# Performance work log

Measured on AMD Instinct MI355X. Metric: run time of the kernel, lower is better.

## Reference

```python
import jax, jax.numpy as jnp
import numpy as np

B, L, V, E, H, C, OUT = 128, 256, 50000, 300, 128, 4, 2
D = 2 * H  # features_size == sequence_max_len (required by the conv kernel width)
FS = (2, 3, 4, 5)


def _p(key, shape, s=0.05):
    return (jax.random.normal(key, shape) * s).astype(jnp.float32)


def setup_inputs() -> dict:
    key = jax.random.key(0)
    ks = jax.random.split(key, 32)
    emb = _p(ks[0], (V, E)).at[0].set(0.0)  # padding_idx=0
    inp = {
        'utterance': jax.random.randint(ks[1], (B, L), 1, V, dtype=jnp.int32),
        'seq_lengths': jnp.full((B,), L, dtype=jnp.int32),
        'emb': emb,
        'w_ih0': _p(ks[2], (2, 3 * H, E)), 'w_hh0': _p(ks[3], (2, 3 * H, H)),
        'b_ih0': _p(ks[4], (2, 3 * H)), 'b_hh0': _p(ks[5], (2, 3 * H)),
        'w_ih1': _p(ks[6], (2, 3 * H, 2 * H)), 'w_hh1': _p(ks[7], (2, 3 * H, H)),
        'b_ih1': _p(ks[8], (2, 3 * H)), 'b_hh1': _p(ks[9], (2, 3 * H)),
        'att_w': _p(ks[10], (C, D, D)), 'att_b': _p(ks[11], (C,)),
        'att_wv2': _p(ks[12], (C, D, D)), 'att_bv': _p(ks[13], (C, D)),
        'att_wv1': _p(ks[14], (C, D)),
        'fc_w': _p(ks[15], (OUT, sum(FS))), 'fc_b': _p(ks[16], (OUT,)),
    }
    for i, fs in enumerate(FS):
        inp[f'conv_w{i}'] = _p(ks[17 + 2 * i], (fs, C, fs, L))
        inp[f'conv_b{i}'] = _p(ks[18 + 2 * i], (fs,))
    return inp


def _gru_dir(x, w_ih, w_hh, b_ih, b_hh, reverse):
    # x: (B,T,in) -> (B,T,H); PyTorch GRU cell equations, eval mode (no dropout)
    gx = jnp.einsum('bti,gi->btg', x, w_ih) + b_ih  # (B,T,3H)

    def step(h, gxt):
        gh = h @ w_hh.T + b_hh
        xr, xz, xn = jnp.split(gxt, 3, axis=-1)
        hr, hz, hn = jnp.split(gh, 3, axis=-1)
        r = jax.nn.sigmoid(xr + hr)
        z = jax.nn.sigmoid(xz + hz)
        n = jnp.tanh(xn + r * hn)
        h = (1.0 - z) * n + z * h
        return h, h

    h0 = jnp.zeros((x.shape[0], w_hh.shape[1]), x.dtype)
    _, ys = jax.lax.scan(step, h0, jnp.swapaxes(gx, 0, 1), reverse=reverse)
    return jnp.swapaxes(ys, 0, 1)


def _bigru_layer(x, w_ih, w_hh, b_ih, b_hh):
    f = _gru_dir(x, w_ih[0], w_hh[0], b_ih[0], b_hh[0], False)
    b = _gru_dir(x, w_ih[1], w_hh[1], b_ih[1], b_hh[1], True)
    return jnp.concatenate([f, b], axis=-1)


def _forward(utterance, emb, w_ih0, w_hh0, b_ih0, b_hh0, w_ih1, w_hh1, b_ih1, b_hh1,
             att_w, att_b, att_wv2, att_bv, att_wv1, conv_params, fc_w, fc_b):
    x = emb[utterance]                                   # (B,L,E)
    x = _bigru_layer(x, w_ih0, w_hh0, b_ih0, b_hh0)      # (B,L,2H)
    x = _bigru_layer(x, w_ih1, w_hh1, b_ih1, b_hh1)      # (B,L,D)
    # --- AMCNN attention, vectorized over channels c ---
    mat = jnp.einsum('bld,cde->cble', x, att_w)          # mat_l per channel (C,B,L,D)
    # M_l[b,i,j] = <inputs[b,i], mat_l[b,j]> + b_l  (the torch tile/sum written as matmul)
    M = jnp.einsum('bid,cbjd->cbij', x, mat) + att_b[:, None, None, None]
    a = jax.nn.softmax(jnp.tanh(M).sum(axis=3), axis=2)  # scalar attention (C,B,L)
    g = jax.nn.sigmoid(jnp.einsum('bld,cde->cble', x, att_wv2) + att_bv[:, None, None, :])
    aa = jax.nn.softmax(jnp.einsum('cble,ce->cbl', g, att_wv1), axis=2)  # vector attn (C,B,L)
    new = jnp.einsum('cbl,bld->cbd', aa, x)              # weighted sum, broadcast over L
    Cf = a[..., None] * x[None] + new[:, :, None, :]     # (C,B,L,D)
    Cf = jnp.transpose(Cf, (1, 0, 2, 3))                 # (B,C,L,D)
    # --- conv blocks: Conv2d(k=(fs,L)) + ReLU + MaxPool((L-fs+1,1)) + Flatten ---
    pools = []
    for w, bi in conv_params:
        y = jax.lax.conv_general_dilated(Cf, w, (1, 1), 'VALID',
                                         dimension_numbers=('NCHW', 'OIHW', 'NCHW'))
        y = jax.nn.relu(y + bi[None, :, None, None])     # (B,fs,L-fs+1,1)
        pools.append(y.max(axis=(2, 3)))                 # (B,fs)
    feats = jnp.concatenate(pools, axis=-1)              # (B,sum(FS))
    return feats @ fc_w.T + fc_b                         # (B,OUT)


def reference(utterance, seq_lengths, emb, w_ih0, w_hh0, b_ih0, b_hh0,
              w_ih1, w_hh1, b_ih1, b_hh1, att_w, att_b, att_wv2, att_bv, att_wv1,
              conv_w0, conv_b0, conv_w1, conv_b1, conv_w2, conv_b2, conv_w3, conv_b3,
              fc_w, fc_b):
    # seq_lengths are all == L, so pack/pad_packed is an identity here
    conv_params = ((conv_w0, conv_b0), (conv_w1, conv_b1), (conv_w2, conv_b2), (conv_w3, conv_b3))
    return _forward(utterance, emb, w_ih0, w_hh0, b_ih0, b_hh0, w_ih1, w_hh1, b_ih1, b_hh1,
                    att_w, att_b, att_wv2, att_bv, att_wv1, conv_params, fc_w, fc_b)
```

## Files before the change

kernel.cpp:

```cpp
#include <hip/hip_runtime.h>
#include <hip/hip_bf16.h>
#include <hip/hip_fp16.h>

#define Bn  128
#define Ln  256
#define En  300
#define Hn  128
#define Cn  4
#define Dn  256
#define G3n 384
#define BLn (Bn * Ln)

typedef __hip_bfloat16 bf16;
typedef short s16x8 __attribute__((ext_vector_type(8)));
typedef float f32x4 __attribute__((ext_vector_type(4)));
typedef _Float16 h16x2 __attribute__((ext_vector_type(2)));

__device__ __forceinline__ float ldf(const float* p) { return *p; }
__device__ __forceinline__ float ldf(const bf16* p)  { return __bfloat162float(*p); }
__device__ __forceinline__ void stf(float* p, float v) { *p = v; }
__device__ __forceinline__ void stf(bf16* p, float v)  { *p = __float2bfloat16(v); }

__device__ __forceinline__ ushort f2bf(float f) {
    bf16 h = __float2bfloat16(f);
    return *reinterpret_cast<ushort*>(&h);
}
__device__ __forceinline__ float bfu(ushort x) {
    unsigned t = ((unsigned)x) << 16;
    return __builtin_bit_cast(float, t);
}

#if __has_builtin(__builtin_amdgcn_fdot2)
__device__ __forceinline__ float dot2f(h16x2 w, h16x2 h, float c) {
    return __builtin_amdgcn_fdot2(w, h, c, false);
}
#else
__device__ __forceinline__ float dot2f(h16x2 w, h16x2 h, float c) {
    return fmaf((float)w[0], (float)h[0], fmaf((float)w[1], (float)h[1], c));
}
#endif
#define BCH(x) __builtin_bit_cast(h16x2, x)

__device__ __forceinline__ float rdl(float v, int l) {
    return __builtin_bit_cast(float,
        __builtin_amdgcn_readlane(__builtin_bit_cast(int, v), l));
}

__device__ __forceinline__ float4 ld4f(const float* p) { return *(const float4*)p; }
__device__ __forceinline__ float4 ld4f(const bf16* p) {
    ushort4 u = *(const ushort4*)p;
    return make_float4(bfu(u.x), bfu(u.y), bfu(u.z), bfu(u.w));
}

template<class AT, class WTp, class OT, bool GATHER, int SM>
__global__ __launch_bounds__(256)
void gemm_mfma(const AT* __restrict__ A, const WTp* __restrict__ W,
               const float* __restrict__ bias, OT* __restrict__ Cout,
               const int* __restrict__ gidx, int M, int N, int K)
{
    __shared__ ushort Asm[128 * 40];
    __shared__ ushort Bsm[128 * 40];
    const int bm = blockIdx.y * 128, bn = blockIdx.x * 128;
    const int tid = threadIdx.x;
    const int lane = tid & 63, w = tid >> 6, wr = w >> 1, wc = w & 1;

    const AT* arow[4];
    const WTp* brow[4];
#pragma unroll
    for (int u = 0; u < 4; ++u) {
        const int idx = tid + u * 256;
        const int m = idx >> 3;
        arow[u] = A + (size_t)(GATHER ? gidx[bm + m] : (bm + m)) * K;
        brow[u] = W + (size_t)(bn + m) * K;
    }

    f32x4 acc[4][4] = {};
    const int nkt = (K + 31) >> 5;
    for (int kt = 0; kt < nkt; ++kt) {
        const int k0 = kt << 5;
#pragma unroll
        for (int u = 0; u < 4; ++u) {
            const int idx = tid + u * 256;
            const int m = idx >> 3, kq = idx & 7;
            const int kb = k0 + kq * 4;
            float4 v, q;
            if (kb + 4 <= K) {
                v = ld4f(arow[u] + kb);
                q = ld4f(brow[u] + kb);
            } else {
                v.x = kb + 0 < K ? ldf(&arow[u][kb + 0]) : 0.f;
                v.y = kb + 1 < K ? ldf(&arow[u][kb + 1]) : 0.f;
                v.z = kb + 2 < K ? ldf(&arow[u][kb + 2]) : 0.f;
                v.w = kb + 3 < K ? ldf(&arow[u][kb + 3]) : 0.f;
                q.x = kb + 0 < K ? ldf(&brow[u][kb + 0]) : 0.f;
                q.y = kb + 1 < K ? ldf(&brow[u][kb + 1]) : 0.f;
                q.z = kb + 2 < K ? ldf(&brow[u][kb + 2]) : 0.f;
                q.w = kb + 3 < K ? ldf(&brow[u][kb + 3]) : 0.f;
            }
            *(ushort4*)&Asm[m * 40 + kq * 4] =
                make_ushort4(f2bf(v.x), f2bf(v.y), f2bf(v.z), f2bf(v.w));
            *(ushort4*)&Bsm[m * 40 + kq * 4] =
                make_ushort4(f2bf(q.x), f2bf(q.y), f2bf(q.z), f2bf(q.w));
        }
        __syncthreads();
        s16x8 af[4], bfr[4];
#pragma unroll
        for (int t = 0; t < 4; ++t) {
            af[t]  = *(const s16x8*)&Asm[(wr * 64 + t * 16 + (lane & 15)) * 40 + (lane >> 4) * 8];
            bfr[t] = *(const s16x8*)&Bsm[(wc * 64 + t * 16 + (lane & 15)) * 40 + (lane >> 4) * 8];
        }
#pragma unroll
        for (int mf = 0; mf < 4; ++mf)
#pragma unroll
            for (int nf = 0; nf < 4; ++nf)
                acc[mf][nf] = __builtin_amdgcn_mfma_f32_16x16x32_bf16(
                    af[mf], bfr[nf], acc[mf][nf], 0, 0, 0);
        __syncthreads();
    }

#pragma unroll
    for (int mf = 0; mf < 4; ++mf)
#pragma unroll
        for (int nf = 0; nf < 4; ++nf) {
            const int col = bn + wc * 64 + nf * 16 + (lane & 15);
            const float bv_ = bias ? bias[col] : 0.f;
#pragma unroll
            for (int i = 0; i < 4; ++i) {
                const int row = bm + wr * 64 + mf * 16 + (lane >> 4) * 4 + i;
                const float v = acc[mf][nf][i] + bv_;
                if (SM == 1)
                    stf(&Cout[((size_t)(row >> 8) * N + col) * 256 + (row & 255)], v);
                else
                    stf(&Cout[(size_t)row * N + col], v);
            }
        }
}

__global__ __launch_bounds__(768, 1)
void gru_scan_v10(const bf16* __restrict__ gx, const float* __restrict__ w_hh,
                  const float* __restrict__ b_hh, bf16* __restrict__ out)
{
    const int b = blockIdx.x, dir = blockIdx.y;
    const int t = threadIdx.x;
    const int half = t >= 384 ? 1 : 0;
    const int r = t - 384 * half;
    const int lane = t & 63;
    __shared__ __align__(16) ushort wl[384 * 136];
    __shared__ __align__(16) ushort hp16[128];
    __shared__ float h_sh[128];
    __shared__ float part[384];
    __shared__ float rs[128], zs[128], gxn[128], ghn[128];

    const float* wbase = w_hh + (size_t)dir * G3n * Hn;
    for (int idx = t; idx < G3n * 64; idx += 768) {
        const int row = idx >> 6, k2 = idx & 63;
        const float2 v = *(const float2*)(wbase + row * Hn + 2 * k2);
        h16x2 p; p[0] = (_Float16)v.x; p[1] = (_Float16)v.y;
        *(h16x2*)&wl[row * 136 + 2 * k2] = p;
    }
    if (t < 128) { hp16[t] = 0; h_sh[t] = 0.f; }
    const float bh = b_hh[dir * G3n + r];
    __syncthreads();

    const size_t g0 = (size_t)b * Ln * 768 + dir * G3n + r
                      + (dir ? (size_t)(Ln - 1) * 768 : 0);
    const long gstep = dir ? -768L : 768L;
    float gcur = 0.f, gnx = 0.f;
    if (!half) { gcur = ldf(&gx[g0]); gnx = ldf(&gx[g0 + gstep]); }

    const ushort* wrow = &wl[r * 136 + half * 64];

    for (int s = 0; s < Ln; ++s) {
        const int tt = dir ? (Ln - 1 - s) : s;
        float gn2 = 0.f;
        if (!half && s + 2 < Ln) gn2 = ldf(&gx[g0 + (long)(s + 2) * gstep]);

        const float4 hown = *(const float4*)&hp16[half * 64 + (lane & 7) * 8];

        float a0 = 0.f, a1 = 0.f, a2 = 0.f, a3 = 0.f;
#pragma unroll
        for (int j = 0; j < 8; ++j) {
            const float4 wv = *(const float4*)&wrow[8 * j];
            a0 = dot2f(BCH(wv.x), BCH(rdl(hown.x, j)), a0);
            a1 = dot2f(BCH(wv.y), BCH(rdl(hown.y, j)), a1);
            a2 = dot2f(BCH(wv.z), BCH(rdl(hown.z, j)), a2);
            a3 = dot2f(BCH(wv.w), BCH(rdl(hown.w, j)), a3);
        }
        const float acc = (a0 + a1) + (a2 + a3);
        if (half) part[r] = acc;
        __syncthreads();

        if (!half) {
            const float tot = acc + part[r] + bh;
            if (r < 128)      rs[r]       = 1.f / (1.f + expf(-(gcur + tot)));
            else if (r < 256) zs[r - 128] = 1.f / (1.f + expf(-(gcur + tot)));
            else { gxn[r - 256] = gcur; ghn[r - 256] = tot; }
        }
        __syncthreads();

        if (t < 128) {
            const int j = t;
            const float nn = tanhf(gxn[j] + rs[j] * ghn[j]);
            const float hnew = (1.f - zs[j]) * nn + zs[j] * h_sh[j];
            h_sh[j] = hnew;
            const _Float16 hf = (_Float16)hnew;
            hp16[j] = __builtin_bit_cast(ushort, hf);
            out[((size_t)b * Ln + tt) * Dn + dir * Hn + j] = __float2bfloat16(hnew);
        }
        __syncthreads();
        if (!half) { gcur = gnx; gnx = gn2; }
    }
}

__global__ __launch_bounds__(256)
void attn_score_mfma(const bf16* __restrict__ x, const bf16* __restrict__ matb,
                     const float* __restrict__ attb, float* __restrict__ sout)
{
    const int it = blockIdx.x, b = blockIdx.y, c = blockIdx.z;
    const bf16* A  = x + ((size_t)b * 256 + it * 128) * 256;
    const bf16* Bm = matb + (size_t)b * 256 * 1024 + c * 256;
    __shared__ ushort Xs[128 * 40];
    __shared__ ushort Ms[128 * 40];
    const int tid = threadIdx.x, lane = tid & 63, w = tid >> 6;
    const float bc = attb[c];
    float psum[2][4] = {};

    for (int jt = 0; jt < 2; ++jt) {
        f32x4 acc[2][8] = {};
        for (int kt = 0; kt < 8; ++kt) {
            const int k0 = kt << 5;
#pragma unroll
            for (int u = 0; u < 2; ++u) {
                const int idx = tid + u * 256;
                const int m = idx >> 2, q = idx & 3;
                *(s16x8*)&Xs[m * 40 + q * 8] =
                    *(const s16x8*)&A[(size_t)m * 256 + k0 + q * 8];
                *(s16x8*)&Ms[m * 40 + q * 8] =
                    *(const s16x8*)&Bm[(size_t)(jt * 128 + m) * 1024 + k0 + q * 8];
            }
            __syncthreads();
            s16x8 af[2], bfr[8];
#pragma unroll
            for (int t = 0; t < 2; ++t)
                af[t] = *(const s16x8*)&Xs[(w * 32 + t * 16 + (lane & 15)) * 40 + (lane >> 4) * 8];
#pragma unroll
            for (int t = 0; t < 8; ++t)
                bfr[t] = *(const s16x8*)&Ms[(t * 16 + (lane & 15)) * 40 + (lane >> 4) * 8];
#pragma unroll
            for (int mf = 0; mf < 2; ++mf)
#pragma unroll
                for (int nf = 0; nf < 8; ++nf)
                    acc[mf][nf] = __builtin_amdgcn_mfma_f32_16x16x32_bf16(
                        af[mf], bfr[nf], acc[mf][nf], 0, 0, 0);
            __syncthreads();
        }
#pragma unroll
        for (int mf = 0; mf < 2; ++mf)
#pragma unroll
            for (int nf = 0; nf < 8; ++nf)
#pragma unroll
                for (int i = 0; i < 4; ++i)
                    psum[mf][i] += tanhf(acc[mf][nf][i] + bc);
    }

#pragma unroll
    for (int mf = 0; mf < 2; ++mf)
#pragma unroll
        for (int i = 0; i < 4; ++i) {
            float v = psum[mf][i];
            v += __shfl_xor(v, 1); v += __shfl_xor(v, 2);
            v += __shfl_xor(v, 4); v += __shfl_xor(v, 8);
            if ((lane & 15) == 0)
                sout[(size_t)c * BLn + b * 256 + it * 128 + w * 32 + mf * 16 + (lane >> 4) * 4 + i] = v;
        }
}

__global__ __launch_bounds__(256)
void gv_reduce(const bf16* __restrict__ gv, const float* __restrict__ bv,
               const float* __restrict__ wv1, float* __restrict__ al)
{
    const int row = blockIdx.x * 4 + (threadIdx.x >> 6);
    const int c = blockIdx.y;
    const int l = threadIdx.x & 63;
    const ushort4 u = *(const ushort4*)&gv[(size_t)row * 1024 + c * 256 + l * 4];
    const float4 bb = *(const float4*)(bv + c * Dn + l * 4);
    const float4 w  = *(const float4*)(wv1 + c * Dn + l * 4);
    float s = w.x / (1.f + expf(-(bfu(u.x) + bb.x)))
            + w.y / (1.f + expf(-(bfu(u.y) + bb.y)))
            + w.z / (1.f + expf(-(bfu(u.z) + bb.z)))
            + w.w / (1.f + expf(-(bfu(u.w) + bb.w)));
#pragma unroll
    for (int m = 1; m < 64; m <<= 1) s += __shfl_xor(s, m);
    if (l == 0) al[(size_t)c * BLn + row] = s;
}

__global__ void transpose256(const float* __restrict__ src, bf16* __restrict__ dst)
{
    const float* s = src + (size_t)blockIdx.x * 65536;
    bf16* d = dst + (size_t)blockIdx.x * 65536;
    __shared__ float t[32][33];
    const int tx = threadIdx.x & 31, ty8 = threadIdx.x >> 5;
    for (int bi = 0; bi < 8; ++bi)
        for (int bj = 0; bj < 8; ++bj) {
            __syncthreads();
            for (int r = ty8; r < 32; r += 8)
                t[r][tx] = s[(size_t)(bi * 32 + r) * 256 + bj * 32 + tx];
            __syncthreads();
            for (int r = ty8; r < 32; r += 8)
                stf(&d[(size_t)(bj * 32 + r) * 256 + bi * 32 + tx], t[tx][r]);
        }
}

__global__ void softmax256(const float* __restrict__ in, float* __restrict__ out)
{
    __shared__ float red[256];
    const int row = blockIdx.x, t = threadIdx.x;
    const float v = in[(size_t)row * 256 + t];
    red[t] = v; __syncthreads();
    for (int off = 128; off; off >>= 1) {
        if (t < off) red[t] = fmaxf(red[t], red[t + off]);
        __syncthreads();
    }
    const float mx = red[0]; __syncthreads();
    const float e = expf(v - mx);
    red[t] = e; __syncthreads();
    for (int off = 128; off; off >>= 1) {
        if (t < off) red[t] += red[t + off];
        __syncthreads();
    }
    out[(size_t)row * 256 + t] = e / red[0];
}

__global__ __launch_bounds__(256)
void weighted_sum_kernel(const float* __restrict__ aa,
                         const bf16* __restrict__ x,
                         float* __restrict__ outnew)
{
    const int b = blockIdx.x, d = threadIdx.x;
    __shared__ float w4[4][Ln];
    for (int i = d; i < 4 * Ln; i += 256)
        w4[i >> 8][i & 255] = aa[((size_t)(i >> 8) * Bn + b) * Ln + (i & 255)];
    __syncthreads();
    float a0 = 0.f, a1 = 0.f, a2 = 0.f, a3 = 0.f;
    for (int l = 0; l < Ln; ++l) {
        const float xv = ldf(&x[((size_t)b * Ln + l) * Dn + d]);
        a0 += w4[0][l] * xv; a1 += w4[1][l] * xv;
        a2 += w4[2][l] * xv; a3 += w4[3][l] * xv;
    }
    outnew[((size_t)0 * Bn + b) * Dn + d] = a0;
    outnew[((size_t)1 * Bn + b) * Dn + d] = a1;
    outnew[((size_t)2 * Bn + b) * Dn + d] = a2;
    outnew[((size_t)3 * Bn + b) * Dn + d] = a3;
}

__global__ void wpack_fill(const float* __restrict__ w0, const float* __restrict__ w1,
                           const float* __restrict__ w2, const float* __restrict__ w3,
                           float* __restrict__ wp)
{
    const int f = blockIdx.x;
    if (f < 4) {
        const int cnt[4]  = {4096, 9216, 16384, 25600};
        const int boff[4] = {0, 4096, 13312, 29696};
        const float* src = f == 0 ? w0 : f == 1 ? w1 : f == 2 ? w2 : w3;
        for (int i = threadIdx.x; i < cnt[f]; i += blockDim.x)
            wp[boff[f] + i] = src[i];
    } else {
        for (int i = threadIdx.x; i < 65536 - 55296; i += blockDim.x)
            wp[55296 + i] = 0.f;
    }
}

__global__ __launch_bounds__(256)
void nwd_kernel(const float* __restrict__ nw, const float* __restrict__ wp,
                float* __restrict__ nwd)
{
    const int b = blockIdx.x;
    __shared__ float ns[4][256];
    for (int i = threadIdx.x; i < 1024; i += 256)
        ns[i >> 8][i & 255] = nw[((size_t)((i >> 8) * Bn + b) << 8) + (i & 255)];
    __syncthreads();
    const int row = threadIdx.x;
    if (row < 216) {
        int f, base;
        if (row < 16)       { f = 0; base = 0; }
        else if (row < 52)  { f = 1; base = 16; }
        else if (row < 116) { f = 2; base = 52; }
        else                { f = 3; base = 116; }
        const int fs = f + 2, local = row - base;
        const int c = (local / fs) & 3;
        const float* wr = wp + (size_t)row * 256;
        float acc = 0.f;
        for (int k = 0; k < 256; ++k) acc += ns[c][k] * wr[k];
        nwd[b * 256 + row] = acc;
    }
}

__global__ __launch_bounds__(256)
void conv_combine(const float* __restrict__ xwT, const float* __restrict__ a,
                  const float* __restrict__ nwd, const float* __restrict__ cb,
                  float* __restrict__ pool, int fs, int base, int poff)
{
    const int b = blockIdx.x, tid = threadIdx.x;
    __shared__ float ash[4][256];
    __shared__ float basev[5];
    __shared__ float red[256];
    for (int i = tid; i < 1024; i += 256)
        ash[i >> 8][i & 255] = a[((size_t)((i >> 8) * Bn + b) << 8) + (i & 255)];
    if (tid < fs) {
        float s = cb[tid];
        for (int c = 0; c < 4; ++c)
            for (int kh = 0; kh < fs; ++kh)
                s += nwd[b * 256 + base + (tid * 4 + c) * fs + kh];
        basev[tid] = s;
    }
    __syncthreads();
    const int ni = Ln - fs + 1;
    const float* xb = xwT + ((size_t)b << 16);
    for (int o = 0; o < fs; ++o) {
        float best = 0.f;
        if (tid < ni) {
            float acc = basev[o];
            for (int c = 0; c < 4; ++c)
                for (int kh = 0; kh < fs; ++kh) {
                    const int row = base + (o * 4 + c) * fs + kh;
                    acc += ash[c][tid + kh] * xb[(row << 8) + tid + kh];
                }
            best = fmaxf(acc, 0.f);
        }
        red[tid] = best; __syncthreads();
        for (int off = 128; off; off >>= 1) {
            if (tid < off) red[tid] = fmaxf(red[tid], red[tid + off]);
            __syncthreads();
        }
        if (tid == 0) pool[b * 14 + poff + o] = red[0];
        __syncthreads();
    }
}

__global__ void fc_kernel(const float* __restrict__ pool, const float* __restrict__ fw,
                          const float* __restrict__ fb, float* __restrict__ out)
{
    const int i = threadIdx.x;
    const int b = i >> 1, o = i & 1;
    float acc = fb[o];
#pragma unroll
    for (int f = 0; f < 14; ++f) acc += pool[b * 14 + f] * fw[o * 14 + f];
    out[i] = acc;
}

extern "C" void kernel_launch(void* const* d_in, const int* in_sizes, int n_in,
                              void* d_out, int out_size, void* d_ws, size_t ws_size,
                              hipStream_t stream)
{
    const int*   utt    = (const int*)  d_in[0];
    const float* emb    = (const float*)d_in[2];
    const float* w_ih0  = (const float*)d_in[3];
    const float* w_hh0  = (const float*)d_in[4];
    const float* b_ih0  = (const float*)d_in[5];
    const float* b_hh0  = (const float*)d_in[6];
    const float* w_ih1  = (const float*)d_in[7];
    const float* w_hh1  = (const float*)d_in[8];
    const float* b_ih1  = (const float*)d_in[9];
    const float* b_hh1  = (const float*)d_in[10];
    const float* att_w  = (const float*)d_in[11];
    const float* att_b  = (const float*)d_in[12];
    const float* att_wv2= (const float*)d_in[13];
    const float* att_bv = (const float*)d_in[14];
    const float* att_wv1= (const float*)d_in[15];
    const float* fc_w   = (const float*)d_in[16];
    const float* fc_b   = (const float*)d_in[17];
    const float* cw[4] = {(const float*)d_in[18], (const float*)d_in[20],
                          (const float*)d_in[22], (const float*)d_in[24]};
    const float* cb[4] = {(const float*)d_in[19], (const float*)d_in[21],
                          (const float*)d_in[23], (const float*)d_in[25]};

    float* ws = (float*)d_ws;
    bf16*  GX   = (bf16*)ws;
    bf16*  H1   = (bf16*)(ws + 12582912);
    bf16*  H2   = (bf16*)(ws + 16777216);
    bf16*  WT   = (bf16*)(ws + 20971520);
    float* WP   = ws + 20971520 + 131072;
    float* S    = WP + 65536;
    float* Aa   = S + 131072;
    float* AL   = Aa + 131072;
    float* AAa  = AL + 131072;
    float* NEW_ = AAa + 131072;
    float* NWD  = NEW_ + 131072;
    float* POOL = NWD + 32768;
    bf16*  MATB = (bf16*)ws;
    float* XWT  = ws;

    gemm_mfma<float, float, bf16, true, 0><<<dim3(6, 256), 256, 0, stream>>>(
        emb, w_ih0, b_ih0, GX, utt, BLn, 768, En);
    gru_scan_v10<<<dim3(Bn, 2), 768, 0, stream>>>(GX, w_hh0, b_hh0, H1);
    gemm_mfma<bf16, float, bf16, false, 0><<<dim3(6, 256), 256, 0, stream>>>(
        H1, w_ih1, b_ih1, GX, nullptr, BLn, 768, Dn);
    gru_scan_v10<<<dim3(Bn, 2), 768, 0, stream>>>(GX, w_hh1, b_hh1, H2);

    transpose256<<<4, 256, 0, stream>>>(att_w, WT);
    gemm_mfma<bf16, bf16, bf16, false, 0><<<dim3(8, 256), 256, 0, stream>>>(
        H2, WT, nullptr, MATB, nullptr, BLn, 1024, Dn);
    attn_score_mfma<<<dim3(2, Bn, Cn), 256, 0, stream>>>(H2, MATB, att_b, S);
    softmax256<<<Cn * Bn, 256, 0, stream>>>(S, Aa);

    transpose256<<<4, 256, 0, stream>>>(att_wv2, WT);
    gemm_mfma<bf16, bf16, bf16, false, 0><<<dim3(8, 256), 256, 0, stream>>>(
        H2, WT, nullptr, MATB, nullptr, BLn, 1024, Dn);
    gv_reduce<<<dim3(BLn / 4, Cn), 256, 0, stream>>>(MATB, att_bv, att_wv1, AL);
    softmax256<<<Cn * Bn, 256, 0, stream>>>(AL, AAa);
    weighted_sum_kernel<<<Bn, 256, 0, stream>>>(AAa, H2, NEW_);

    wpack_fill<<<5, 256, 0, stream>>>(cw[0], cw[1], cw[2], cw[3], WP);
    gemm_mfma<bf16, float, float, false, 1><<<dim3(2, 256), 256, 0, stream>>>(
        H2, WP, nullptr, XWT, nullptr, BLn, Dn, Dn);
    nwd_kernel<<<Bn, 256, 0, stream>>>(NEW_, WP, NWD);

    const int baserow[4] = {0, 16, 52, 116};
    const int poff[4]    = {0, 2, 5, 9};
    for (int f = 0; f < 4; ++f)
        conv_combine<<<Bn, 256, 0, stream>>>(XWT, Aa, NWD, cb[f], POOL, f + 2, baserow[f], poff[f]);

    fc_kernel<<<1, 256, 0, stream>>>(POOL, fc_w, fc_b, (float*)d_out);
}
```

Baseline: 1.175 ms.

## Fuse value-attention GEMM with sigmoid reduction, bf16 conv intermediate, LDS h reads in GRU

Replaces the separate value-attention GEMM plus gv_reduce with one kernel that applies bias, sigmoid and the wv1 weighting to the accumulators. Partial sums are reduced across lanes and atomically added into a zeroed buffer, so the large bf16 intermediate matrix is never written or read back. The conv projection output is stored as bf16 instead of float to halve its traffic. The GRU scan now reads h directly from shared memory instead of using readlane broadcasts. Risks are atomic ordering nondeterminism and reduced precision in the conv path.

```diff
diff --git a/kernel.cpp b/kernel.cpp
--- a/kernel.cpp
+++ b/kernel.cpp
@@ -40,11 +40,6 @@
 }
 #endif
 #define BCH(x) __builtin_bit_cast(h16x2, x)
-
-__device__ __forceinline__ float rdl(float v, int l) {
-    return __builtin_bit_cast(float,
-        __builtin_amdgcn_readlane(__builtin_bit_cast(int, v), l));
-}
 
 __device__ __forceinline__ float4 ld4f(const float* p) { return *(const float4*)p; }
 __device__ __forceinline__ float4 ld4f(const bf16* p) {
@@ -136,15 +131,78 @@
         }
 }
 
+__global__ __launch_bounds__(256)
+void gv_gemm_reduce(const bf16* __restrict__ A, const bf16* __restrict__ W,
+                    const float* __restrict__ bv, const float* __restrict__ wv1,
+                    float* __restrict__ al)
+{
+    __shared__ ushort Asm[128 * 40];
+    __shared__ ushort Bsm[128 * 40];
+    const int bm = blockIdx.y * 128, bn = blockIdx.x * 128;
+    const int tid = threadIdx.x;
+    const int lane = tid & 63, w = tid >> 6, wr = w >> 1, wc = w & 1;
+
+    f32x4 acc[4][4] = {};
+    for (int kt = 0; kt < 8; ++kt) {
+        const int k0 = kt << 5;
+#pragma unroll
+        for (int u = 0; u < 2; ++u) {
+            const int idx = tid + u * 256;
+            const int m = idx >> 2, q = idx & 3;
+            *(s16x8*)&Asm[m * 40 + q * 8] =
+                *(const s16x8*)&A[(size_t)(bm + m) * 256 + k0 + q * 8];
+            *(s16x8*)&Bsm[m * 40 + q * 8] =
+                *(const s16x8*)&W[(size_t)(bn + m) * 256 + k0 + q * 8];
+        }
+        __syncthreads();
+        s16x8 af[4], bfr[4];
+#pragma unroll
+        for (int t = 0; t < 4; ++t) {
+            af[t]  = *(const s16x8*)&Asm[(wr * 64 + t * 16 + (lane & 15)) * 40 + (lane >> 4) * 8];
+            bfr[t] = *(const s16x8*)&Bsm[(wc * 64 + t * 16 + (lane & 15)) * 40 + (lane >> 4) * 8];
+        }
+#pragma unroll
+        for (int mf = 0; mf < 4; ++mf)
+#pragma unroll
+            for (int nf = 0; nf < 4; ++nf)
+                acc[mf][nf] = __builtin_amdgcn_mfma_f32_16x16x32_bf16(
+                    af[mf], bfr[nf], acc[mf][nf], 0, 0, 0);
+        __syncthreads();
+    }
+
+    float bb[4], wv[4];
+#pragma unroll
+    for (int nf = 0; nf < 4; ++nf) {
+        const int col = bn + wc * 64 + nf * 16 + (lane & 15);
+        bb[nf] = bv[col];
+        wv[nf] = wv1[col];
+    }
+    const size_t cbase = (size_t)(bn >> 8) * BLn;
+#pragma unroll
+    for (int mf = 0; mf < 4; ++mf)
+#pragma unroll
+        for (int i = 0; i < 4; ++i) {
+            float p = 0.f;
+#pragma unroll
+            for (int nf = 0; nf < 4; ++nf)
+                p += wv[nf] / (1.f + expf(-(acc[mf][nf][i] + bb[nf])));
+            p += __shfl_xor(p, 1); p += __shfl_xor(p, 2);
+            p += __shfl_xor(p, 4); p += __shfl_xor(p, 8);
+            if ((lane & 15) == 0) {
+                const int row = bm + wr * 64 + mf * 16 + (lane >> 4) * 4 + i;
+                atomicAdd(&al[cbase + row], p);
+            }
+        }
+}
+
 __global__ __launch_bounds__(768, 1)
-void gru_scan_v10(const bf16* __restrict__ gx, const float* __restrict__ w_hh,
-                  const float* __restrict__ b_hh, bf16* __restrict__ out)
+void gru_scan_v9(const bf16* __restrict__ gx, const float* __restrict__ w_hh,
+                 const float* __restrict__ b_hh, bf16* __restrict__ out)
 {
     const int b = blockIdx.x, dir = blockIdx.y;
     const int t = threadIdx.x;
     const int half = t >= 384 ? 1 : 0;
     const int r = t - 384 * half;
-    const int lane = t & 63;
     __shared__ __align__(16) ushort wl[384 * 136];
     __shared__ __align__(16) ushort hp16[128];
     __shared__ float h_sh[128];
@@ -168,23 +226,23 @@
     float gcur = 0.f, gnx = 0.f;
     if (!half) { gcur = ldf(&gx[g0]); gnx = ldf(&gx[g0 + gstep]); }
 
-    const ushort* wrow = &wl[r * 136 + half * 64];
+    const ushort* wrow  = &wl[r * 136 + half * 64];
+    const ushort* hbase = &hp16[half * 64];
 
     for (int s = 0; s < Ln; ++s) {
         const int tt = dir ? (Ln - 1 - s) : s;
         float gn2 = 0.f;
         if (!half && s + 2 < Ln) gn2 = ldf(&gx[g0 + (long)(s + 2) * gstep]);
 
-        const float4 hown = *(const float4*)&hp16[half * 64 + (lane & 7) * 8];
-
         float a0 = 0.f, a1 = 0.f, a2 = 0.f, a3 = 0.f;
 #pragma unroll
         for (int j = 0; j < 8; ++j) {
             const float4 wv = *(const float4*)&wrow[8 * j];
-            a0 = dot2f(BCH(wv.x), BCH(rdl(hown.x, j)), a0);
-            a1 = dot2f(BCH(wv.y), BCH(rdl(hown.y, j)), a1);
-            a2 = dot2f(BCH(wv.z), BCH(rdl(hown.z, j)), a2);
-            a3 = dot2f(BCH(wv.w), BCH(rdl(hown.w, j)), a3);
+            const float4 hv = *(const float4*)&hbase[8 * j];
+            a0 = dot2f(BCH(wv.x), BCH(hv.x), a0);
+            a1 = dot2f(BCH(wv.y), BCH(hv.y), a1);
+            a2 = dot2f(BCH(wv.z), BCH(hv.z), a2);
+            a3 = dot2f(BCH(wv.w), BCH(hv.w), a3);
         }
         const float acc = (a0 + a1) + (a2 + a3);
         if (half) part[r] = acc;
@@ -273,25 +331,6 @@
             if ((lane & 15) == 0)
                 sout[(size_t)c * BLn + b * 256 + it * 128 + w * 32 + mf * 16 + (lane >> 4) * 4 + i] = v;
         }
-}
-
-__global__ __launch_bounds__(256)
-void gv_reduce(const bf16* __restrict__ gv, const float* __restrict__ bv,
-               const float* __restrict__ wv1, float* __restrict__ al)
-{
-    const int row = blockIdx.x * 4 + (threadIdx.x >> 6);
-    const int c = blockIdx.y;
-    const int l = threadIdx.x & 63;
-    const ushort4 u = *(const ushort4*)&gv[(size_t)row * 1024 + c * 256 + l * 4];
-    const float4 bb = *(const float4*)(bv + c * Dn + l * 4);
-    const float4 w  = *(const float4*)(wv1 + c * Dn + l * 4);
-    float s = w.x / (1.f + expf(-(bfu(u.x) + bb.x)))
-            + w.y / (1.f + expf(-(bfu(u.y) + bb.y)))
-            + w.z / (1.f + expf(-(bfu(u.z) + bb.z)))
-            + w.w / (1.f + expf(-(bfu(u.w) + bb.w)));
-#pragma unroll
-    for (int m = 1; m < 64; m <<= 1) s += __shfl_xor(s, m);
-    if (l == 0) al[(size_t)c * BLn + row] = s;
 }
 
 __global__ void transpose256(const float* __restrict__ src, bf16* __restrict__ dst)
@@ -396,7 +435,7 @@
 }
 
 __global__ __launch_bounds__(256)
-void conv_combine(const float* __restrict__ xwT, const float* __restrict__ a,
+void conv_combine(const bf16* __restrict__ xwT, const float* __restrict__ a,
                   const float* __restrict__ nwd, const float* __restrict__ cb,
                   float* __restrict__ pool, int fs, int base, int poff)
 {
@@ -415,7 +454,7 @@
     }
     __syncthreads();
     const int ni = Ln - fs + 1;
-    const float* xb = xwT + ((size_t)b << 16);
+    const bf16* xb = xwT + ((size_t)b << 16);
     for (int o = 0; o < fs; ++o) {
         float best = 0.f;
         if (tid < ni) {
@@ -423,7 +462,7 @@
             for (int c = 0; c < 4; ++c)
                 for (int kh = 0; kh < fs; ++kh) {
                     const int row = base + (o * 4 + c) * fs + kh;
-                    acc += ash[c][tid + kh] * xb[(row << 8) + tid + kh];
+                    acc += ash[c][tid + kh] * ldf(&xb[(row << 8) + tid + kh]);
                 }
             best = fmaxf(acc, 0.f);
         }
@@ -488,14 +527,14 @@
     float* NWD  = NEW_ + 131072;
     float* POOL = NWD + 32768;
     bf16*  MATB = (bf16*)ws;
-    float* XWT  = ws;
+    bf16*  XWT  = (bf16*)ws;
 
     gemm_mfma<float, float, bf16, true, 0><<<dim3(6, 256), 256, 0, stream>>>(
         emb, w_ih0, b_ih0, GX, utt, BLn, 768, En);
-    gru_scan_v10<<<dim3(Bn, 2), 768, 0, stream>>>(GX, w_hh0, b_hh0, H1);
+    gru_scan_v9<<<dim3(Bn, 2), 768, 0, stream>>>(GX, w_hh0, b_hh0, H1);
     gemm_mfma<bf16, float, bf16, false, 0><<<dim3(6, 256), 256, 0, stream>>>(
         H1, w_ih1, b_ih1, GX, nullptr, BLn, 768, Dn);
-    gru_scan_v10<<<dim3(Bn, 2), 768, 0, stream>>>(GX, w_hh1, b_hh1, H2);
+    gru_scan_v9<<<dim3(Bn, 2), 768, 0, stream>>>(GX, w_hh1, b_hh1, H2);
 
     transpose256<<<4, 256, 0, stream>>>(att_w, WT);
     gemm_mfma<bf16, bf16, bf16, false, 0><<<dim3(8, 256), 256, 0, stream>>>(
@@ -504,14 +543,13 @@
     softmax256<<<Cn * Bn, 256, 0, stream>>>(S, Aa);
 
     transpose256<<<4, 256, 0, stream>>>(att_wv2, WT);
-    gemm_mfma<bf16, bf16, bf16, false, 0><<<dim3(8, 256), 256, 0, stream>>>(
-        H2, WT, nullptr, MATB, nullptr, BLn, 1024, Dn);
-    gv_reduce<<<dim3(BLn / 4, Cn), 256, 0, stream>>>(MATB, att_bv, att_wv1, AL);
+    hipMemsetAsync(AL, 0, (size_t)Cn * BLn * sizeof(float), stream);
+    gv_gemm_reduce<<<dim3(8, 256), 256, 0, stream>>>(H2, WT, att_bv, att_wv1, AL);
     softmax256<<<Cn * Bn, 256, 0, stream>>>(AL, AAa);
     weighted_sum_kernel<<<Bn, 256, 0, stream>>>(AAa, H2, NEW_);
 
     wpack_fill<<<5, 256, 0, stream>>>(cw[0], cw[1], cw[2], cw[3], WP);
-    gemm_mfma<bf16, float, float, false, 1><<<dim3(2, 256), 256, 0, stream>>>(
+    gemm_mfma<bf16, float, bf16, false, 1><<<dim3(2, 256), 256, 0, stream>>>(
         H2, WP, nullptr, XWT, nullptr, BLn, Dn, Dn);
     nwd_kernel<<<Bn, 256, 0, stream>>>(NEW_, WP, NWD);
 
```

Result: faster. 1.096 ms (-6.7%).
